# Kernel tuning notes

Measured on AMD Instinct MI355X. Metric: run time of the kernel, lower is better.

## Reference

```python
import jax, jax.numpy as jnp
import numpy as np

EMB = 1024
HEADS = 16
HD = EMB // HEADS
EPS = 1e-5

def _ln(x, g, b):
    m = jnp.mean(x, axis=-1, keepdims=True)
    v = jnp.mean((x - m) ** 2, axis=-1, keepdims=True)
    return (x - m) * jax.lax.rsqrt(v + EPS) * g + b

def setup_inputs() -> dict:
    key = jax.random.key(0)
    ks = jax.random.split(key, 12)
    s_in = 1.0 / np.sqrt(EMB)
    s_ff = 1.0 / np.sqrt(4 * EMB)
    return {
        "x": jax.random.normal(ks[0], (2, 2048, EMB), jnp.float32),
        "wq": jax.random.uniform(ks[1], (HEADS, EMB, HD), jnp.float32, -s_in, s_in),
        "wk": jax.random.uniform(ks[2], (HEADS, EMB, HD), jnp.float32, -s_in, s_in),
        "wv": jax.random.uniform(ks[3], (HEADS, EMB, HD), jnp.float32, -s_in, s_in),
        "wo": jax.random.uniform(ks[4], (EMB, EMB), jnp.float32, -s_in, s_in),
        "bo": jax.random.uniform(ks[5], (EMB,), jnp.float32, -s_in, s_in),
        "g1": jnp.ones((EMB,), jnp.float32),
        "b1": jnp.zeros((EMB,), jnp.float32),
        "g2": jnp.ones((EMB,), jnp.float32),
        "b2": jnp.zeros((EMB,), jnp.float32),
        "w1": jax.random.uniform(ks[6], (EMB, 4 * EMB), jnp.float32, -s_in, s_in),
        "bf1": jax.random.uniform(ks[7], (4 * EMB,), jnp.float32, -s_in, s_in),
        "w2": jax.random.uniform(ks[8], (4 * EMB, EMB), jnp.float32, -s_ff, s_ff),
        "bf2": jax.random.uniform(ks[9], (EMB,), jnp.float32, -s_ff, s_ff),
    }

def reference(x, wq, wk, wv, wo, bo, g1, b1, g2, b2, w1, bf1, w2, bf2):
    B, T, C = x.shape
    h = _ln(x, g1, b1)
    # all heads batched: [B,H,T,HD]
    q = jnp.einsum('btc,hcd->bhtd', h, wq)
    k = jnp.einsum('btc,hcd->bhtd', h, wk)
    v = jnp.einsum('btc,hcd->bhtd', h, wv)
    # NOTE: original scales by full emb_size C**-0.5, not head_size
    scores = jnp.einsum('bhtd,bhsd->bhts', q, k) * (C ** -0.5)
    causal = jnp.tril(jnp.ones((T, T), bool))
    scores = jnp.where(causal, scores, -jnp.inf)
    w = jax.nn.softmax(scores, axis=-1)
    attn = jnp.einsum('bhts,bhsd->bhtd', w, v)
    attn = attn.transpose(0, 2, 1, 3).reshape(B, T, C)  # concat heads
    x = x + attn @ wo + bo
    h2 = _ln(x, g2, b2)
    ffn = jax.nn.relu(h2 @ w1 + bf1) @ w2 + bf2
    return x + ffn
```

## Files before the change

kernel.cpp:

```cpp
#include <hip/hip_runtime.h>

typedef __bf16 bf16x8 __attribute__((ext_vector_type(8)));
typedef float f32x4 __attribute__((ext_vector_type(4)));
typedef short s16x8 __attribute__((ext_vector_type(8)));

#define DEV __device__ __forceinline__

DEV float b2f(unsigned short u) {
  unsigned int x = ((unsigned int)u) << 16;
  return __builtin_bit_cast(float, x);
}
DEV unsigned short f2b(float f) {
  unsigned int x = __builtin_bit_cast(unsigned int, f);
  x += 0x7fffu + ((x >> 16) & 1u);
  return (unsigned short)(x >> 16);
}
DEV f32x4 mfma16(bf16x8 a, bf16x8 b, f32x4 c) {
  return __builtin_amdgcn_mfma_f32_16x16x32_bf16(a, b, c, 0, 0, 0);
}
DEV void gl2lds16(const unsigned short* g, unsigned short* l) {
  __builtin_amdgcn_global_load_lds(
      (const __attribute__((address_space(1))) void*)g,
      (__attribute__((address_space(3))) void*)l, 16, 0, 0);
}

__global__ __launch_bounds__(256)
void transpose_k(const float* __restrict__ in, unsigned short* __restrict__ out,
                 int K, int N, long zin, long zout) {
  __shared__ float tile[32][33];
  in  += (size_t)blockIdx.z * zin;
  out += (size_t)blockIdx.z * zout;
  int n0 = blockIdx.x * 32, k0 = blockIdx.y * 32;
  int tx = threadIdx.x, ty = threadIdx.y;
  #pragma unroll
  for (int i = ty; i < 32; i += 8)
    tile[i][tx] = in[(size_t)(k0 + i) * N + n0 + tx];
  __syncthreads();
  #pragma unroll
  for (int i = ty; i < 32; i += 8)
    out[(size_t)(n0 + i) * K + k0 + tx] = f2b(tile[tx][i]);
}

__global__ __launch_bounds__(256)
void vtrans_k(const unsigned short* __restrict__ qkv, unsigned short* __restrict__ vT) {
  __shared__ unsigned short tile[32][33];
  int bh = blockIdx.z, b = bh >> 4, h = bh & 15;
  int t0 = blockIdx.x * 32, d0 = blockIdx.y * 32;
  const unsigned short* in = qkv + (size_t)b * 2048 * 3072 + 2048 + h * 64;
  unsigned short* out = vT + (size_t)bh * 64 * 2048;
  int tx = threadIdx.x, ty = threadIdx.y;
  #pragma unroll
  for (int i = ty; i < 32; i += 8)
    tile[i][tx] = in[(size_t)(t0 + i) * 3072 + d0 + tx];
  __syncthreads();
  #pragma unroll
  for (int i = ty; i < 32; i += 8)
    out[(size_t)(d0 + i) * 2048 + t0 + tx] = tile[tx][i];
}

__global__ __launch_bounds__(256)
void ln_kernel(const float* __restrict__ x, const float* __restrict__ g,
               const float* __restrict__ b, unsigned short* __restrict__ o) {
  __shared__ float rs[4];
  __shared__ float rq[4];
  int row = blockIdx.x, tid = threadIdx.x;
  const float* xr = x + (size_t)row * 1024;
  float4 raw = ((const float4*)xr)[tid];
  float s = raw.x + raw.y + raw.z + raw.w;
  float q = raw.x*raw.x + raw.y*raw.y + raw.z*raw.z + raw.w*raw.w;
  #pragma unroll
  for (int off = 32; off > 0; off >>= 1) {
    s += __shfl_down(s, off);
    q += __shfl_down(q, off);
  }
  int wave = tid >> 6;
  if ((tid & 63) == 0) { rs[wave] = s; rq[wave] = q; }
  __syncthreads();
  float ts = rs[0] + rs[1] + rs[2] + rs[3];
  float tq = rq[0] + rq[1] + rq[2] + rq[3];
  float mean = ts * (1.0f/1024.0f);
  float var = tq * (1.0f/1024.0f) - mean*mean;
  float rstd = rsqrtf(var + 1e-5f);
  float4 gr = ((const float4*)g)[tid];
  float4 br = ((const float4*)b)[tid];
  float o0 = (raw.x-mean)*rstd*gr.x + br.x;
  float o1 = (raw.y-mean)*rstd*gr.y + br.y;
  float o2 = (raw.z-mean)*rstd*gr.z + br.z;
  float o3 = (raw.w-mean)*rstd*gr.w + br.w;
  uint2 ov;
  ov.x = (unsigned int)f2b(o0) | ((unsigned int)f2b(o1) << 16);
  ov.y = (unsigned int)f2b(o2) | ((unsigned int)f2b(o3) << 16);
  ((uint2*)(o + (size_t)row * 1024))[tid] = ov;
}

template<bool RELU, bool BIAS, bool RESID, bool OUTF32>
__global__ __launch_bounds__(256)
void gemm_bt(const unsigned short* __restrict__ A, const unsigned short* __restrict__ Bt,
             const float* __restrict__ bias, const float* __restrict__ resid,
             void* __restrict__ Cv, int M, int N, int K) {
  __shared__ unsigned short As[2][128*32];
  __shared__ unsigned short Bs[2][128*32];
  const int tid = threadIdx.x;
  const int lane = tid & 63;
  const int quad = lane >> 4, l16 = lane & 15;
  const int wave = tid >> 6;
  const int m0 = blockIdx.y * 128, n0 = blockIdx.x * 128;
  const int wm = (wave >> 1) * 64, wn = (wave & 1) * 64;

  f32x4 acc[4][4];
  #pragma unroll
  for (int i = 0; i < 4; ++i)
    #pragma unroll
    for (int j = 0; j < 4; ++j) acc[i][j] = (f32x4){0.f, 0.f, 0.f, 0.f};

  const int srow = tid >> 2;
  const int scol = (tid & 3) * 8;
  const unsigned short* Ab = A + (size_t)m0 * K;
  const unsigned short* Bb = Bt + (size_t)n0 * K;

  auto stage = [&](int buf, int k0) {
    gl2lds16(Ab + (size_t)srow * K + k0 + scol,        &As[buf][tid * 8]);
    gl2lds16(Ab + (size_t)(srow + 64) * K + k0 + scol, &As[buf][2048 + tid * 8]);
    gl2lds16(Bb + (size_t)srow * K + k0 + scol,        &Bs[buf][tid * 8]);
    gl2lds16(Bb + (size_t)(srow + 64) * K + k0 + scol, &Bs[buf][2048 + tid * 8]);
  };

  const int niter = K >> 5;
  stage(0, 0);
  __syncthreads();

  for (int it = 0; it < niter; ++it) {
    const int buf = it & 1;
    if (it + 1 < niter) stage(buf ^ 1, (it + 1) * 32);
    bf16x8 af[4], bfr[4];
    #pragma unroll
    for (int i = 0; i < 4; ++i)
      af[i] = __builtin_bit_cast(bf16x8, *(const s16x8*)&As[buf][(wm + i*16 + l16)*32 + quad*8]);
    #pragma unroll
    for (int j = 0; j < 4; ++j)
      bfr[j] = __builtin_bit_cast(bf16x8, *(const s16x8*)&Bs[buf][(wn + j*16 + l16)*32 + quad*8]);
    #pragma unroll
    for (int i = 0; i < 4; ++i)
      #pragma unroll
      for (int j = 0; j < 4; ++j)
        acc[i][j] = mfma16(af[i], bfr[j], acc[i][j]);
    __syncthreads();
  }

  #pragma unroll
  for (int i = 0; i < 4; ++i) {
    const int row = m0 + wm + i*16 + quad*4;
    #pragma unroll
    for (int j = 0; j < 4; ++j) {
      const int col = n0 + wn + j*16 + l16;
      float bv = 0.f;
      if (BIAS) bv = bias[col];
      #pragma unroll
      for (int r = 0; r < 4; ++r) {
        float v = acc[i][j][r] + bv;
        if (RESID) v += resid[(size_t)(row + r) * N + col];
        if (RELU) v = fmaxf(v, 0.f);
        if (OUTF32) ((float*)Cv)[(size_t)(row + r) * N + col] = v;
        else ((unsigned short*)Cv)[(size_t)(row + r) * N + col] = f2b(v);
      }
    }
  }
}

__global__ __launch_bounds__(256)
void gemm_n1024(const unsigned short* __restrict__ A, const unsigned short* __restrict__ Bt,
                const float* __restrict__ bias, const float* __restrict__ resid,
                float* __restrict__ C, int M, int N, int K) {
  __shared__ unsigned short As[2][64*64];
  __shared__ unsigned short Bs[2][128*64];
  const int tid = threadIdx.x;
  const int lane = tid & 63;
  const int quad = lane >> 4, l16 = lane & 15;
  const int wave = tid >> 6;
  const int id = blockIdx.x;
  const int xcd = id & 7, i2 = id >> 3;
  const int mt = (xcd << 3) | (i2 >> 3);
  const int nt = i2 & 7;
  const int m0 = mt * 64, n0 = nt * 128;
  const int wm = (wave >> 1) * 32, wn = (wave & 1) * 64;

  f32x4 acc[2][4];
  #pragma unroll
  for (int i = 0; i < 2; ++i)
    #pragma unroll
    for (int j = 0; j < 4; ++j) acc[i][j] = (f32x4){0.f, 0.f, 0.f, 0.f};

  const int srow = tid >> 3;
  const int scc  = ((tid & 7) ^ (srow & 7)) * 8;
  const unsigned short* Ab = A + (size_t)m0 * K;
  const unsigned short* Bb = Bt + (size_t)n0 * K;

  auto stage = [&](int buf, int k0) {
    gl2lds16(Ab + (size_t)srow * K + k0 + scc,         &As[buf][tid * 8]);
    gl2lds16(Ab + (size_t)(srow + 32) * K + k0 + scc,  &As[buf][2048 + tid * 8]);
    gl2lds16(Bb + (size_t)srow * K + k0 + scc,         &Bs[buf][tid * 8]);
    gl2lds16(Bb + (size_t)(srow + 32) * K + k0 + scc,  &Bs[buf][2048 + tid * 8]);
    gl2lds16(Bb + (size_t)(srow + 64) * K + k0 + scc,  &Bs[buf][4096 + tid * 8]);
    gl2lds16(Bb + (size_t)(srow + 96) * K + k0 + scc,  &Bs[buf][6144 + tid * 8]);
  };

  const int niter = K >> 6;
  stage(0, 0);
  __syncthreads();

  for (int it = 0; it < niter; ++it) {
    const int buf = it & 1;
    if (it + 1 < niter) stage(buf ^ 1, (it + 1) * 64);
    #pragma unroll
    for (int s = 0; s < 2; ++s) {
      bf16x8 af[2], bfr[4];
      #pragma unroll
      for (int i = 0; i < 2; ++i) {
        const int R = wm + i*16 + l16;
        af[i] = __builtin_bit_cast(bf16x8,
          *(const s16x8*)&As[buf][R*64 + (((s*4 + quad) ^ (R & 7)) * 8)]);
      }
      #pragma unroll
      for (int j = 0; j < 4; ++j) {
        const int R = wn + j*16 + l16;
        bfr[j] = __builtin_bit_cast(bf16x8,
          *(const s16x8*)&Bs[buf][R*64 + (((s*4 + quad) ^ (R & 7)) * 8)]);
      }
      #pragma unroll
      for (int i = 0; i < 2; ++i)
        #pragma unroll
        for (int j = 0; j < 4; ++j)
          acc[i][j] = mfma16(af[i], bfr[j], acc[i][j]);
    }
    __syncthreads();
  }

  #pragma unroll
  for (int i = 0; i < 2; ++i) {
    const int row = m0 + wm + i*16 + quad*4;
    #pragma unroll
    for (int j = 0; j < 4; ++j) {
      const int col = n0 + wn + j*16 + l16;
      const float bv = bias[col];
      #pragma unroll
      for (int r = 0; r < 4; ++r)
        C[(size_t)(row + r) * N + col] = acc[i][j][r] + bv + resid[(size_t)(row + r) * N + col];
    }
  }
}

__global__ __launch_bounds__(256)
void attn_kernel(const unsigned short* __restrict__ qkv,
                 const unsigned short* __restrict__ vT,
                 unsigned short* __restrict__ outc) {
  __shared__ unsigned short Ks[2][64*64];
  __shared__ unsigned short Vs[2][64*64];
  __shared__ unsigned short Ps[2][4*16*72];
  const int tid = threadIdx.x, lane = tid & 63, wave = tid >> 6;
  const int quad = lane >> 4, l16 = lane & 15;
  const int bh = blockIdx.y, b = bh >> 4, h = bh & 15;
  const int jA = blockIdx.x, jB = 31 - jA;
  const size_t tokbase = (size_t)b * 2048 * 3072;
  const unsigned short* Q  = qkv + tokbase + h * 64;
  const unsigned short* Kg = qkv + tokbase + 1024 + h * 64;
  const unsigned short* Vg = vT + (size_t)bh * 64 * 2048;

  bf16x8 qf[2][2];
  #pragma unroll
  for (int t = 0; t < 2; ++t) {
    const int qrow = (t ? jB : jA) * 64 + wave * 16 + l16;
    #pragma unroll
    for (int s = 0; s < 2; ++s) {
      s16x8 raw = *(const s16x8*)(Q + (size_t)qrow * 3072 + s * 32 + quad * 8);
      unsigned short* rp = (unsigned short*)&raw;
      #pragma unroll
      for (int j = 0; j < 8; ++j) rp[j] = f2b(b2f(rp[j]) * 0.03125f);
      qf[t][s] = __builtin_bit_cast(bf16x8, raw);
    }
  }

  f32x4 accO[2][4];
  #pragma unroll
  for (int t = 0; t < 2; ++t)
    #pragma unroll
    for (int i = 0; i < 4; ++i) accO[t][i] = (f32x4){0.f, 0.f, 0.f, 0.f};
  float lrow[2][4] = {{0.f,0.f,0.f,0.f},{0.f,0.f,0.f,0.f}};

  const int r8 = lane >> 3;
  const int cs = (((lane & 7) ^ r8) * 8);

  auto stage = [&](int buf, int kv0) {
    #pragma unroll
    for (int i = 0; i < 2; ++i) {
      int row = wave * 16 + i * 8;
      gl2lds16(Kg + (size_t)(kv0 + row + r8) * 3072 + cs, &Ks[buf][row * 64 + lane * 8]);
      gl2lds16(Vg + (size_t)(row + r8) * 2048 + kv0 + cs, &Vs[buf][row * 64 + lane * 8]);
    }
  };

  const int ntile = jB + 1;
  stage(0, 0);
  __syncthreads();

  for (int it = 0; it < ntile; ++it) {
    const int buf = it & 1;
    if (it + 1 < ntile) stage(buf ^ 1, (it + 1) * 64);

    #pragma unroll
    for (int t = 0; t < 2; ++t) {
      const int jT = t ? jB : jA;
      if (it > jT) continue;
      f32x4 sv[4];
      #pragma unroll
      for (int ni = 0; ni < 4; ++ni) {
        sv[ni] = (f32x4){0.f, 0.f, 0.f, 0.f};
        #pragma unroll
        for (int s = 0; s < 2; ++s) {
          bf16x8 kf = __builtin_bit_cast(bf16x8,
            *(const s16x8*)&Ks[buf][(ni*16 + l16)*64 + (((s*4 + quad) ^ (l16 & 7)) * 8)]);
          sv[ni] = mfma16(qf[t][s], kf, sv[ni]);
        }
      }
      if (it == jT) {
        const int rowg = jT*64 + wave*16 + quad*4;
        const int kv0 = it * 64;
        #pragma unroll
        for (int ni = 0; ni < 4; ++ni) {
          const int colg = kv0 + ni*16 + l16;
          #pragma unroll
          for (int r = 0; r < 4; ++r)
            if (colg > rowg + r) sv[ni][r] = -__builtin_inff();
        }
      }
      float rsum[4] = {0.f, 0.f, 0.f, 0.f};
      unsigned short pb[4][4];
      #pragma unroll
      for (int ni = 0; ni < 4; ++ni)
        #pragma unroll
        for (int r = 0; r < 4; ++r) {
          float p = __expf(sv[ni][r]);
          rsum[r] += p;
          pb[ni][r] = f2b(p);
        }
      #pragma unroll
      for (int r = 0; r < 4; ++r) {
        float s2 = rsum[r];
        s2 += __shfl_xor(s2, 1);
        s2 += __shfl_xor(s2, 2);
        s2 += __shfl_xor(s2, 4);
        s2 += __shfl_xor(s2, 8);
        lrow[t][r] += s2;
      }
      #pragma unroll
      for (int ni = 0; ni < 4; ++ni)
        #pragma unroll
        for (int r = 0; r < 4; ++r)
          Ps[t][wave*1152 + (quad*4 + r)*72 + ni*16 + l16] = pb[ni][r];
      __asm__ volatile("s_waitcnt lgkmcnt(0)" ::: "memory");
      #pragma unroll
      for (int s = 0; s < 2; ++s) {
        bf16x8 pf = __builtin_bit_cast(bf16x8,
          *(const s16x8*)&Ps[t][wave*1152 + l16*72 + s*32 + quad*8]);
        #pragma unroll
        for (int ni = 0; ni < 4; ++ni) {
          bf16x8 vf = __builtin_bit_cast(bf16x8,
            *(const s16x8*)&Vs[buf][(ni*16 + l16)*64 + (((s*4 + quad) ^ (l16 & 7)) * 8)]);
          accO[t][ni] = mfma16(pf, vf, accO[t][ni]);
        }
      }
    }
    __syncthreads();
  }

  #pragma unroll
  for (int t = 0; t < 2; ++t) {
    const int rowg = (t ? jB : jA)*64 + wave*16 + quad*4;
    #pragma unroll
    for (int ni = 0; ni < 4; ++ni)
      #pragma unroll
      for (int r = 0; r < 4; ++r) {
        float o = accO[t][ni][r] / lrow[t][r];
        outc[(size_t)(b*2048 + rowg + r) * 1024 + h*64 + ni*16 + l16] = f2b(o);
      }
  }
}

extern "C" void kernel_launch(void* const* d_in, const int* in_sizes, int n_in,
                              void* d_out, int out_size, void* d_ws, size_t ws_size,
                              hipStream_t stream) {
  (void)in_sizes; (void)n_in; (void)out_size; (void)ws_size;
  const float* x   = (const float*)d_in[0];
  const float* wq  = (const float*)d_in[1];
  const float* wk  = (const float*)d_in[2];
  const float* wv  = (const float*)d_in[3];
  const float* wo  = (const float*)d_in[4];
  const float* bo  = (const float*)d_in[5];
  const float* g1  = (const float*)d_in[6];
  const float* b1  = (const float*)d_in[7];
  const float* g2  = (const float*)d_in[8];
  const float* b2  = (const float*)d_in[9];
  const float* w1  = (const float*)d_in[10];
  const float* bf1 = (const float*)d_in[11];
  const float* w2  = (const float*)d_in[12];
  const float* bf2 = (const float*)d_in[13];
  float* out = (float*)d_out;

  unsigned short* ws    = (unsigned short*)d_ws;
  unsigned short* wqkvt = ws;
  unsigned short* wot   = wqkvt + 3*1024*1024;
  unsigned short* w1t   = wot   + 1024*1024;
  unsigned short* w2t   = w1t   + 4096*1024;
  unsigned short* hbuf  = w2t   + 4096*1024;
  unsigned short* qkvb  = hbuf  + 4096*1024;
  unsigned short* attnb = qkvb  + (size_t)4096*3072;
  float*          x2b   = (float*)(attnb + 4096*1024);
  unsigned short* vTb   = (unsigned short*)x2b;
  unsigned short* midb  = qkvb;

  dim3 tb(32, 8);
  transpose_k<<<dim3(2,32,16), tb, 0, stream>>>(wq, wqkvt,             1024, 64, 65536, 65536);
  transpose_k<<<dim3(2,32,16), tb, 0, stream>>>(wk, wqkvt + 1024*1024, 1024, 64, 65536, 65536);
  transpose_k<<<dim3(2,32,16), tb, 0, stream>>>(wv, wqkvt + 2048*1024, 1024, 64, 65536, 65536);
  transpose_k<<<dim3(32,32,1),  tb, 0, stream>>>(wo, wot, 1024, 1024, 0, 0);
  transpose_k<<<dim3(128,32,1), tb, 0, stream>>>(w1, w1t, 1024, 4096, 0, 0);
  transpose_k<<<dim3(32,128,1), tb, 0, stream>>>(w2, w2t, 4096, 1024, 0, 0);

  ln_kernel<<<4096, 256, 0, stream>>>(x, g1, b1, hbuf);
  gemm_bt<false,false,false,false><<<dim3(24,32), 256, 0, stream>>>(hbuf, wqkvt, nullptr, nullptr, qkvb, 4096, 3072, 1024);
  vtrans_k<<<dim3(64,2,32), tb, 0, stream>>>(qkvb, vTb);
  attn_kernel<<<dim3(16,32), 256, 0, stream>>>(qkvb, vTb, attnb);
  gemm_n1024<<<512, 256, 0, stream>>>(attnb, wot, bo, x, x2b, 4096, 1024, 1024);
  ln_kernel<<<4096, 256, 0, stream>>>(x2b, g2, b2, hbuf);
  gemm_bt<true,true,false,false><<<dim3(32,32), 256, 0, stream>>>(hbuf, w1t, bf1, nullptr, midb, 4096, 4096, 1024);
  gemm_n1024<<<512, 256, 0, stream>>>(midb, w2t, bf2, x2b, out, 4096, 1024, 4096);
}
```

Before: 366.5 us.

## Fuse V transpose into QKV GEMM, merge weight transposes, MFMA row sums

The QKV GEMM epilogue now writes the V columns directly in transposed [b,h,d,t] layout, which removes the separate vtrans kernel and its extra pass over V. The three Q/K/V weight transposes become a single launch. In attention, the per-row softmax sum is computed with an extra MFMA against a vector of ones instead of shuffle reductions, the P buffer is single-buffered, and the final divide becomes a reciprocal multiply. Packed bf16 conversion is used in layernorm and when building P. Row sums now come from bf16-rounded probabilities, which changes numerics slightly, and the transposed V stores from the GEMM epilogue are 8-byte scattered writes.

Result: faster. 343.7 us (-6.2%).

```diff
diff --git a/kernel.cpp b/kernel.cpp
--- a/kernel.cpp
+++ b/kernel.cpp
@@ -1,4 +1,5 @@
 #include <hip/hip_runtime.h>
+#include <hip/hip_bf16.h>
 
 typedef __bf16 bf16x8 __attribute__((ext_vector_type(8)));
 typedef float f32x4 __attribute__((ext_vector_type(4)));
@@ -14,6 +15,13 @@
   unsigned int x = __builtin_bit_cast(unsigned int, f);
   x += 0x7fffu + ((x >> 16) & 1u);
   return (unsigned short)(x >> 16);
+}
+DEV unsigned int f2b2(float a, float b) {
+  float2 t; t.x = a; t.y = b;
+  __hip_bfloat162 v = __float22bfloat162_rn(t);
+  unsigned int r;
+  __builtin_memcpy(&r, &v, 4);
+  return r;
 }
 DEV f32x4 mfma16(bf16x8 a, bf16x8 b, f32x4 c) {
   return __builtin_amdgcn_mfma_f32_16x16x32_bf16(a, b, c, 0, 0, 0);
@@ -42,20 +50,23 @@
 }
 
 __global__ __launch_bounds__(256)
-void vtrans_k(const unsigned short* __restrict__ qkv, unsigned short* __restrict__ vT) {
-  __shared__ unsigned short tile[32][33];
-  int bh = blockIdx.z, b = bh >> 4, h = bh & 15;
-  int t0 = blockIdx.x * 32, d0 = blockIdx.y * 32;
-  const unsigned short* in = qkv + (size_t)b * 2048 * 3072 + 2048 + h * 64;
-  unsigned short* out = vT + (size_t)bh * 64 * 2048;
+void transpose_qkv(const float* __restrict__ wq, const float* __restrict__ wk,
+                   const float* __restrict__ wv, unsigned short* __restrict__ out) {
+  __shared__ float tile[32][33];
+  const int z = blockIdx.z;
+  const float* in = (z < 16) ? (wq + (size_t)z * 65536)
+                  : (z < 32) ? (wk + (size_t)(z - 16) * 65536)
+                             : (wv + (size_t)(z - 32) * 65536);
+  unsigned short* o = out + (size_t)z * 65536;
+  int n0 = blockIdx.x * 32, k0 = blockIdx.y * 32;
   int tx = threadIdx.x, ty = threadIdx.y;
   #pragma unroll
   for (int i = ty; i < 32; i += 8)
-    tile[i][tx] = in[(size_t)(t0 + i) * 3072 + d0 + tx];
+    tile[i][tx] = in[(size_t)(k0 + i) * 64 + n0 + tx];
   __syncthreads();
   #pragma unroll
   for (int i = ty; i < 32; i += 8)
-    out[(size_t)(d0 + i) * 2048 + t0 + tx] = tile[tx][i];
+    o[(size_t)(n0 + i) * 1024 + k0 + tx] = f2b(tile[tx][i]);
 }
 
 __global__ __launch_bounds__(256)
@@ -88,16 +99,16 @@
   float o2 = (raw.z-mean)*rstd*gr.z + br.z;
   float o3 = (raw.w-mean)*rstd*gr.w + br.w;
   uint2 ov;
-  ov.x = (unsigned int)f2b(o0) | ((unsigned int)f2b(o1) << 16);
-  ov.y = (unsigned int)f2b(o2) | ((unsigned int)f2b(o3) << 16);
+  ov.x = f2b2(o0, o1);
+  ov.y = f2b2(o2, o3);
   ((uint2*)(o + (size_t)row * 1024))[tid] = ov;
 }
 
-template<bool RELU, bool BIAS, bool RESID, bool OUTF32>
+template<bool RELU, bool BIAS, bool RESID, bool OUTF32, bool VFUSE>
 __global__ __launch_bounds__(256)
 void gemm_bt(const unsigned short* __restrict__ A, const unsigned short* __restrict__ Bt,
              const float* __restrict__ bias, const float* __restrict__ resid,
-             void* __restrict__ Cv, int M, int N, int K) {
+             void* __restrict__ Cv, unsigned short* __restrict__ vT, int M, int N, int K) {
   __shared__ unsigned short As[2][128*32];
   __shared__ unsigned short Bs[2][128*32];
   const int tid = threadIdx.x;
@@ -145,6 +156,26 @@
       for (int j = 0; j < 4; ++j)
         acc[i][j] = mfma16(af[i], bfr[j], acc[i][j]);
     __syncthreads();
+  }
+
+  if (VFUSE && n0 >= 2048) {
+    #pragma unroll
+    for (int i = 0; i < 4; ++i) {
+      const int row = m0 + wm + i*16 + quad*4;
+      const int b = row >> 11, tloc = row & 2047;
+      #pragma unroll
+      for (int j = 0; j < 4; ++j) {
+        const int col = n0 + wn + j*16 + l16;
+        const int h = (col - 2048) >> 6, d = col & 63;
+        ushort4 pk;
+        pk.x = f2b(acc[i][j][0]);
+        pk.y = f2b(acc[i][j][1]);
+        pk.z = f2b(acc[i][j][2]);
+        pk.w = f2b(acc[i][j][3]);
+        *(ushort4*)&vT[((size_t)((b*16 + h)*64 + d))*2048 + tloc] = pk;
+      }
+    }
+    return;
   }
 
   #pragma unroll
@@ -255,7 +286,7 @@
                  unsigned short* __restrict__ outc) {
   __shared__ unsigned short Ks[2][64*64];
   __shared__ unsigned short Vs[2][64*64];
-  __shared__ unsigned short Ps[2][4*16*72];
+  __shared__ unsigned short Ps[4*16*72];
   const int tid = threadIdx.x, lane = tid & 63, wave = tid >> 6;
   const int quad = lane >> 4, l16 = lane & 15;
   const int bh = blockIdx.y, b = bh >> 4, h = bh & 15;
@@ -265,6 +296,9 @@
   const unsigned short* Kg = qkv + tokbase + 1024 + h * 64;
   const unsigned short* Vg = vT + (size_t)bh * 64 * 2048;
 
+  const s16x8 ones_s = {0x3F80, 0x3F80, 0x3F80, 0x3F80, 0x3F80, 0x3F80, 0x3F80, 0x3F80};
+  const bf16x8 onesf = __builtin_bit_cast(bf16x8, ones_s);
+
   bf16x8 qf[2][2];
   #pragma unroll
   for (int t = 0; t < 2; ++t) {
@@ -280,11 +314,11 @@
   }
 
   f32x4 accO[2][4];
+  f32x4 accS[2] = {(f32x4){0.f,0.f,0.f,0.f}, (f32x4){0.f,0.f,0.f,0.f}};
   #pragma unroll
   for (int t = 0; t < 2; ++t)
     #pragma unroll
     for (int i = 0; i < 4; ++i) accO[t][i] = (f32x4){0.f, 0.f, 0.f, 0.f};
-  float lrow[2][4] = {{0.f,0.f,0.f,0.f},{0.f,0.f,0.f,0.f}};
 
   const int r8 = lane >> 3;
   const int cs = (((lane & 7) ^ r8) * 8);
@@ -332,35 +366,26 @@
             if (colg > rowg + r) sv[ni][r] = -__builtin_inff();
         }
       }
-      float rsum[4] = {0.f, 0.f, 0.f, 0.f};
-      unsigned short pb[4][4];
-      #pragma unroll
-      for (int ni = 0; ni < 4; ++ni)
-        #pragma unroll
-        for (int r = 0; r < 4; ++r) {
-          float p = __expf(sv[ni][r]);
-          rsum[r] += p;
-          pb[ni][r] = f2b(p);
-        }
-      #pragma unroll
-      for (int r = 0; r < 4; ++r) {
-        float s2 = rsum[r];
-        s2 += __shfl_xor(s2, 1);
-        s2 += __shfl_xor(s2, 2);
-        s2 += __shfl_xor(s2, 4);
-        s2 += __shfl_xor(s2, 8);
-        lrow[t][r] += s2;
-      }
-      #pragma unroll
-      for (int ni = 0; ni < 4; ++ni)
-        #pragma unroll
-        for (int r = 0; r < 4; ++r)
-          Ps[t][wave*1152 + (quad*4 + r)*72 + ni*16 + l16] = pb[ni][r];
+      #pragma unroll
+      for (int ni = 0; ni < 4; ++ni) {
+        float p0 = __expf(sv[ni][0]);
+        float p1 = __expf(sv[ni][1]);
+        float p2 = __expf(sv[ni][2]);
+        float p3 = __expf(sv[ni][3]);
+        unsigned int u01 = f2b2(p0, p1);
+        unsigned int u23 = f2b2(p2, p3);
+        const int base = wave*1152 + ni*16 + l16;
+        Ps[base + (quad*4 + 0)*72] = (unsigned short)u01;
+        Ps[base + (quad*4 + 1)*72] = (unsigned short)(u01 >> 16);
+        Ps[base + (quad*4 + 2)*72] = (unsigned short)u23;
+        Ps[base + (quad*4 + 3)*72] = (unsigned short)(u23 >> 16);
+      }
       __asm__ volatile("s_waitcnt lgkmcnt(0)" ::: "memory");
       #pragma unroll
       for (int s = 0; s < 2; ++s) {
         bf16x8 pf = __builtin_bit_cast(bf16x8,
-          *(const s16x8*)&Ps[t][wave*1152 + l16*72 + s*32 + quad*8]);
+          *(const s16x8*)&Ps[wave*1152 + l16*72 + s*32 + quad*8]);
+        accS[t] = mfma16(pf, onesf, accS[t]);
         #pragma unroll
         for (int ni = 0; ni < 4; ++ni) {
           bf16x8 vf = __builtin_bit_cast(bf16x8,
@@ -375,13 +400,15 @@
   #pragma unroll
   for (int t = 0; t < 2; ++t) {
     const int rowg = (t ? jB : jA)*64 + wave*16 + quad*4;
+    float inv[4];
+    #pragma unroll
+    for (int r = 0; r < 4; ++r) inv[r] = __builtin_amdgcn_rcpf(accS[t][r]);
     #pragma unroll
     for (int ni = 0; ni < 4; ++ni)
       #pragma unroll
-      for (int r = 0; r < 4; ++r) {
-        float o = accO[t][ni][r] / lrow[t][r];
-        outc[(size_t)(b*2048 + rowg + r) * 1024 + h*64 + ni*16 + l16] = f2b(o);
-      }
+      for (int r = 0; r < 4; ++r)
+        outc[(size_t)(b*2048 + rowg + r) * 1024 + h*64 + ni*16 + l16]
+          = f2b(accO[t][ni][r] * inv[r]);
   }
 }
 
@@ -418,19 +445,18 @@
   unsigned short* midb  = qkvb;
 
   dim3 tb(32, 8);
-  transpose_k<<<dim3(2,32,16), tb, 0, stream>>>(wq, wqkvt,             1024, 64, 65536, 65536);
-  transpose_k<<<dim3(2,32,16), tb, 0, stream>>>(wk, wqkvt + 1024*1024, 1024, 64, 65536, 65536);
-  transpose_k<<<dim3(2,32,16), tb, 0, stream>>>(wv, wqkvt + 2048*1024, 1024, 64, 65536, 65536);
+  transpose_qkv<<<dim3(2,32,48), tb, 0, stream>>>(wq, wk, wv, wqkvt);
   transpose_k<<<dim3(32,32,1),  tb, 0, stream>>>(wo, wot, 1024, 1024, 0, 0);
   transpose_k<<<dim3(128,32,1), tb, 0, stream>>>(w1, w1t, 1024, 4096, 0, 0);
   transpose_k<<<dim3(32,128,1), tb, 0, stream>>>(w2, w2t, 4096, 1024, 0, 0);
 
   ln_kernel<<<4096, 256, 0, stream>>>(x, g1, b1, hbuf);
-  gemm_bt<false,false,false,false><<<dim3(24,32), 256, 0, stream>>>(hbuf, wqkvt, nullptr, nullptr, qkvb, 4096, 3072, 1024);
-  vtrans_k<<<dim3(64,2,32), tb, 0, stream>>>(qkvb, vTb);
+  gemm_bt<false,false,false,false,true><<<dim3(24,32), 256, 0, stream>>>(
+      hbuf, wqkvt, nullptr, nullptr, qkvb, vTb, 4096, 3072, 1024);
   attn_kernel<<<dim3(16,32), 256, 0, stream>>>(qkvb, vTb, attnb);
   gemm_n1024<<<512, 256, 0, stream>>>(attnb, wot, bo, x, x2b, 4096, 1024, 1024);
   ln_kernel<<<4096, 256, 0, stream>>>(x2b, g2, b2, hbuf);
-  gemm_bt<true,true,false,false><<<dim3(32,32), 256, 0, stream>>>(hbuf, w1t, bf1, nullptr, midb, 4096, 4096, 1024);
+  gemm_bt<true,true,false,false,false><<<dim3(32,32), 256, 0, stream>>>(
+      hbuf, w1t, bf1, nullptr, midb, nullptr, 4096, 4096, 1024);
   gemm_n1024<<<512, 256, 0, stream>>>(midb, w2t, bf2, x2b, out, 4096, 1024, 4096);
 }
```
